# Optimization experiments

Measured on AMD Instinct MI355X. Metric: run time of the kernel, lower is better.

The kernel has to match this reference:

```python
import jax, jax.numpy as jnp
import numpy as np

D = 512; NH = 8; FF = 2048; LE = 6; LD = 6; V = 97; SM = 512; SQ = 128; B = 16
EPS = 1e-5


def _posenc(length, depth):
    half = depth // 2
    pos = jnp.arange(length, dtype=jnp.float32)[:, None]
    dep = jnp.arange(half, dtype=jnp.float32)[None, :] / half
    ang = pos / (10000.0 ** dep)
    return jnp.concatenate([jnp.sin(ang), jnp.cos(ang)], axis=-1)  # [length, depth]


def _ln(x, w, b):
    mu = jnp.mean(x, axis=-1, keepdims=True)
    var = jnp.mean((x - mu) ** 2, axis=-1, keepdims=True)
    return (x - mu) * jax.lax.rsqrt(var + EPS) * w + b


def _heads(t, S, Bt):
    return t.reshape(S, Bt * NH, D // NH).transpose(1, 0, 2)  # [B*H, S, dk]


def _self_attn(x, wqkv, bqkv, wo, bo, causal):
    S, Bt, _ = x.shape
    qkv = x @ wqkv.T + bqkv
    q, k, v = jnp.split(qkv, 3, axis=-1)
    q = _heads(q, S, Bt); k = _heads(k, S, Bt); v = _heads(v, S, Bt)
    scores = jnp.einsum('hqd,hkd->hqk', q, k) / jnp.sqrt(jnp.asarray(D // NH, x.dtype))
    if causal:
        mask = jnp.triu(jnp.ones((S, S), bool), 1)
        scores = jnp.where(mask[None], -jnp.inf, scores)
    attn = jax.nn.softmax(scores, axis=-1)
    out = jnp.einsum('hqk,hkd->hqd', attn, v).transpose(1, 0, 2).reshape(S, Bt, D)
    return out @ wo.T + bo


def _cross_attn(query, memory, wq, bq, wk, bk, wv, bv, wo, bo):
    Sq, Bt, _ = query.shape
    Sm = memory.shape[0]
    q = _heads(query @ wq.T + bq, Sq, Bt)
    k = _heads(memory @ wk.T + bk, Sm, Bt)
    v = _heads(memory @ wv.T + bv, Sm, Bt)
    scores = jnp.einsum('hqd,hkd->hqk', q, k) / jnp.sqrt(jnp.asarray(D // NH, query.dtype))
    attn = jax.nn.softmax(scores, axis=-1)
    out = jnp.einsum('hqk,hkd->hqd', attn, v).transpose(1, 0, 2).reshape(Sq, Bt, D)
    return out @ wo.T + bo


def _forward(src, tokens, tok_emb,
             enc_qkv_w, enc_qkv_b, enc_out_w, enc_out_b,
             enc_l1_w, enc_l1_b, enc_l2_w, enc_l2_b,
             enc_n1_w, enc_n1_b, enc_n2_w, enc_n2_b,
             dec_qkv_w, dec_qkv_b, dec_sout_w, dec_sout_b,
             dec_q_w, dec_q_b, dec_k_w, dec_k_b, dec_v_w, dec_v_b,
             dec_cout_w, dec_cout_b,
             dec_l1_w, dec_l1_b, dec_l2_w, dec_l2_b,
             dec_n1_w, dec_n1_b, dec_n2_w, dec_n2_b, dec_n3_w, dec_n3_b,
             out_w, out_b):
    # ---- encoder ----
    x = src  # [SM, B, D]
    for i in range(LE):
        x2 = _self_attn(x, enc_qkv_w[i], enc_qkv_b[i], enc_out_w[i], enc_out_b[i], causal=False)
        x = _ln(x + x2, enc_n1_w[i], enc_n1_b[i])
        x2 = jax.nn.relu(x @ enc_l1_w[i].T + enc_l1_b[i]) @ enc_l2_w[i].T + enc_l2_b[i]
        x = _ln(x + x2, enc_n2_w[i], enc_n2_b[i])
    memory = x
    # ---- decoder ----
    tgt = tok_emb[tokens] + _posenc(tokens.shape[0], D)[:, None, :]  # [SQ, B, D]
    for i in range(LD):
        x2 = _self_attn(tgt, dec_qkv_w[i], dec_qkv_b[i], dec_sout_w[i], dec_sout_b[i], causal=True)
        tgt = _ln(tgt + x2, dec_n1_w[i], dec_n1_b[i])
        x2 = _cross_attn(tgt, memory, dec_q_w[i], dec_q_b[i], dec_k_w[i], dec_k_b[i],
                         dec_v_w[i], dec_v_b[i], dec_cout_w[i], dec_cout_b[i])
        tgt = _ln(tgt + x2, dec_n2_w[i], dec_n2_b[i])
        x2 = jax.nn.relu(tgt @ dec_l1_w[i].T + dec_l1_b[i]) @ dec_l2_w[i].T + dec_l2_b[i]
        tgt = _ln(tgt + x2, dec_n3_w[i], dec_n3_b[i])
    return tgt @ out_w.T + out_b  # [SQ, B, V]


def setup_inputs() -> dict:
    key = jax.random.key(0)
    ks = iter(jax.random.split(key, 64))
    g = lambda shape: jax.random.normal(next(ks), shape, dtype=jnp.float32) * 0.02
    inp = {
        'src': jax.random.normal(next(ks), (SM, B, D), dtype=jnp.float32),
        'tokens': jax.random.randint(next(ks), (SQ, B), 0, V),
        'tok_emb': g((V, D)),
        'enc_qkv_w': g((LE, 3 * D, D)), 'enc_qkv_b': g((LE, 3 * D)),
        'enc_out_w': g((LE, D, D)), 'enc_out_b': g((LE, D)),
        'enc_l1_w': g((LE, FF, D)), 'enc_l1_b': g((LE, FF)),
        'enc_l2_w': g((LE, D, FF)), 'enc_l2_b': g((LE, D)),
        'enc_n1_w': jnp.ones((LE, D)), 'enc_n1_b': jnp.zeros((LE, D)),
        'enc_n2_w': jnp.ones((LE, D)), 'enc_n2_b': jnp.zeros((LE, D)),
        'dec_qkv_w': g((LD, 3 * D, D)), 'dec_qkv_b': g((LD, 3 * D)),
        'dec_sout_w': g((LD, D, D)), 'dec_sout_b': g((LD, D)),
        'dec_q_w': g((LD, D, D)), 'dec_q_b': g((LD, D)),
        'dec_k_w': g((LD, D, D)), 'dec_k_b': g((LD, D)),
        'dec_v_w': g((LD, D, D)), 'dec_v_b': g((LD, D)),
        'dec_cout_w': g((LD, D, D)), 'dec_cout_b': g((LD, D)),
        'dec_l1_w': g((LD, FF, D)), 'dec_l1_b': g((LD, FF)),
        'dec_l2_w': g((LD, D, FF)), 'dec_l2_b': g((LD, D)),
        'dec_n1_w': jnp.ones((LD, D)), 'dec_n1_b': jnp.zeros((LD, D)),
        'dec_n2_w': jnp.ones((LD, D)), 'dec_n2_b': jnp.zeros((LD, D)),
        'dec_n3_w': jnp.ones((LD, D)), 'dec_n3_b': jnp.zeros((LD, D)),
        'out_w': g((V, D)), 'out_b': g((V,)),
    }
    return inp


def reference(src, tokens, tok_emb,
              enc_qkv_w, enc_qkv_b, enc_out_w, enc_out_b,
              enc_l1_w, enc_l1_b, enc_l2_w, enc_l2_b,
              enc_n1_w, enc_n1_b, enc_n2_w, enc_n2_b,
              dec_qkv_w, dec_qkv_b, dec_sout_w, dec_sout_b,
              dec_q_w, dec_q_b, dec_k_w, dec_k_b, dec_v_w, dec_v_b,
              dec_cout_w, dec_cout_b,
              dec_l1_w, dec_l1_b, dec_l2_w, dec_l2_b,
              dec_n1_w, dec_n1_b, dec_n2_w, dec_n2_b, dec_n3_w, dec_n3_b,
              out_w, out_b):
    return _forward(src, tokens, tok_emb,
                    enc_qkv_w, enc_qkv_b, enc_out_w, enc_out_b,
                    enc_l1_w, enc_l1_b, enc_l2_w, enc_l2_b,
                    enc_n1_w, enc_n1_b, enc_n2_w, enc_n2_b,
                    dec_qkv_w, dec_qkv_b, dec_sout_w, dec_sout_b,
                    dec_q_w, dec_q_b, dec_k_w, dec_k_b, dec_v_w, dec_v_b,
                    dec_cout_w, dec_cout_b,
                    dec_l1_w, dec_l1_b, dec_l2_w, dec_l2_b,
                    dec_n1_w, dec_n1_b, dec_n2_w, dec_n2_b, dec_n3_w, dec_n3_b,
                    out_w, out_b)
```

## Files before the change

### kernel.cpp

```cpp
#include <hip/hip_runtime.h>
#include <hip/hip_bf16.h>
#include <cstddef>
#include <cstdint>

#define D_MODEL 512
#define BATCH 16
#define EPS_LN 1e-5f

typedef __bf16 bf16x8 __attribute__((ext_vector_type(8)));
typedef float f32x4 __attribute__((ext_vector_type(4)));
typedef unsigned short u16x8 __attribute__((ext_vector_type(8)));
typedef unsigned short u16x4 __attribute__((ext_vector_type(4)));
typedef unsigned short u16x2 __attribute__((ext_vector_type(2)));

__device__ __forceinline__ void gload_lds16(const void* g, void* l) {
    __builtin_amdgcn_global_load_lds(
        (const __attribute__((address_space(1))) void*)g,
        (__attribute__((address_space(3))) void*)l,
        16, 0, 0);
}

template <int BM, int OUTBF16>
__global__ __launch_bounds__(256) void gemm_mfma(
    const __bf16* __restrict__ A, const __bf16* __restrict__ W,
    const float* __restrict__ bias, const float* __restrict__ bias2,
    int bsplit, void* __restrict__ Cout, int N, int M, int K, int relu)
{
    constexpr int WC     = (BM == 128) ? 2 : 4;
    constexpr int WSPAN  = 128 / WC;
    constexpr int NC     = WSPAN / 16;
    constexpr int ABYTES = BM * 128;
    constexpr int PA     = ABYTES / 4096;
    constexpr int BUFB   = ABYTES + 16384;

    __shared__ __align__(16) char smem[2 * BUFB];

    const int tid  = threadIdx.x;
    const int lane = tid & 63;
    const int wid  = tid >> 6;
    const int wrow = (BM == 128) ? (wid >> 1) : 0;
    const int wcol = (BM == 128) ? (wid & 1) : wid;
    const int row0 = blockIdx.y * BM;
    const int col0 = blockIdx.x * 128;

    const int lrow  = lane & 15;
    const int lhalf = lane >> 4;
    const int koff0 = ((lhalf) ^ (lrow & 7)) * 16;
    const int koff1 = ((4 + lhalf) ^ (lrow & 7)) * 16;

    const int srow = tid >> 3;
    const int slot = tid & 7;
    const int sg   = slot ^ (srow & 7);

    f32x4 acc[4][NC] = {};

    const __bf16* Abase = A + (size_t)(row0 + srow) * K + sg * 8;
    const __bf16* Wbase = W + (size_t)(col0 + srow) * K + sg * 8;

    auto stage = [&](char* buf, int kt) {
#pragma unroll
        for (int p = 0; p < PA; ++p)
            gload_lds16(Abase + (size_t)p * 32 * K + kt, buf + p * 4096 + tid * 16);
#pragma unroll
        for (int p = 0; p < 4; ++p)
            gload_lds16(Wbase + (size_t)p * 32 * K + kt,
                        buf + ABYTES + p * 4096 + tid * 16);
    };

    stage(smem, 0);
    const int nkt = K >> 6;
    int cur = 0;
    for (int kt = 0; kt < nkt; ++kt) {
        __syncthreads();
        if (kt + 1 < nkt) stage(smem + (cur ^ 1) * BUFB, (kt + 1) * 64);
        const char* aB = smem + cur * BUFB + (wrow * 64 + lrow) * 128;
        const char* wB = smem + cur * BUFB + ABYTES + (wcol * WSPAN + lrow) * 128;
#pragma unroll
        for (int ks = 0; ks < 2; ++ks) {
            const int ko = ks ? koff1 : koff0;
            bf16x8 af[4], bfr[NC];
#pragma unroll
            for (int m = 0; m < 4; ++m) af[m]  = *(const bf16x8*)(aB + m * 2048 + ko);
#pragma unroll
            for (int n = 0; n < NC; ++n) bfr[n] = *(const bf16x8*)(wB + n * 2048 + ko);
#pragma unroll
            for (int m = 0; m < 4; ++m)
#pragma unroll
                for (int n = 0; n < NC; ++n)
                    acc[m][n] = __builtin_amdgcn_mfma_f32_16x16x32_bf16(
                        af[m], bfr[n], acc[m][n], 0, 0, 0);
        }
        cur ^= 1;
    }

    const int orow = row0 + wrow * 64 + lhalf * 4;
    const int ocol = col0 + wcol * WSPAN + lrow;
#pragma unroll
    for (int n = 0; n < NC; ++n) {
        const int c = ocol + n * 16;
        if (c < M) {
            const float bv = (bias2 && c >= bsplit) ? bias2[c - bsplit] : bias[c];
#pragma unroll
            for (int m = 0; m < 4; ++m) {
#pragma unroll
                for (int j = 0; j < 4; ++j) {
                    const int r = orow + m * 16 + j;
                    float v = acc[m][n][j] + bv;
                    if (relu) v = fmaxf(v, 0.f);
                    if (OUTBF16) ((__bf16*)Cout)[(size_t)r * M + c] = (__bf16)v;
                    else         ((float*)Cout)[(size_t)r * M + c] = v;
                }
            }
        }
    }
}

__global__ __launch_bounds__(256) void transpose_v(
    const __bf16* __restrict__ V, __bf16* __restrict__ VT,
    int stride, int voff, int S)
{
    __shared__ __align__(16) char smem[8192];
    const int tid = threadIdx.x;
    const int kc = blockIdx.x, h = blockIdx.y, b = blockIdx.z;
    const int srow = tid >> 3, slot = tid & 7;
#pragma unroll
    for (int p = 0; p < 2; ++p) {
        int r = p * 32 + srow;
        const __bf16* src = V + ((size_t)(kc * 64 + r) * BATCH + b) * stride
                              + voff + h * 64 + slot * 8;
        gload_lds16(src, smem + (p * 256 + tid) * 16);
    }
    __syncthreads();
    const int l = tid & 63, w = tid >> 6;
    const int d2 = w * 8 + (l >> 3);
    const int s0 = (l & 7) * 8;
    unsigned rows[8];
#pragma unroll
    for (int e = 0; e < 8; ++e)
        rows[e] = *(const unsigned*)(smem + (s0 + e) * 128 + d2 * 4);
    union { __bf16 h8[8]; u16x8 u; } r0, r1;
#pragma unroll
    for (int e = 0; e < 8; ++e) {
        r0.h8[e] = ((const __bf16*)&rows[e])[0];
        r1.h8[e] = ((const __bf16*)&rows[e])[1];
    }
    size_t obase = ((size_t)(b * 8 + h) * 64 + d2 * 2) * S + kc * 64 + s0;
    *(u16x8*)(VT + obase)     = r0.u;
    *(u16x8*)(VT + obase + S) = r1.u;
}

template <int CAUSAL>
__global__ __launch_bounds__(256) void attn_mfma(
    const __bf16* __restrict__ Qb, const __bf16* __restrict__ Kb,
    const __bf16* __restrict__ VT, __bf16* __restrict__ Op,
    int Skv, int qstride, int kstride, int koff, float scale)
{
    __shared__ __align__(16) char smem[40960];
    const int tid = threadIdx.x;
    const int l   = tid & 63;
    const int w   = tid >> 6;
    char* Psm = smem + 32768 + w * 2048;

    const int qc = blockIdx.x;
    const int h  = blockIdx.y;
    const int b  = blockIdx.z;
    const int l15 = l & 15;
    const int g   = l >> 4;
    const int sw  = l15 & 7;

    const int sq = qc * 64 + w * 16 + l15;
    const __bf16* qrow = Qb + ((size_t)sq * BATCH + b) * qstride + h * 64 + g * 8;
    const bf16x8 qf0 = *(const bf16x8*)(qrow);
    const bf16x8 qf1 = *(const bf16x8*)(qrow + 32);

    const int srow = tid >> 3;
    const int slot = tid & 7;

    auto stageKV = [&](char* buf, int kc) {
#pragma unroll
        for (int p = 0; p < 2; ++p) {
            const int r   = p * 32 + srow;
            const int sgo = (slot ^ (r & 7)) * 8;
            const __bf16* ksrc = Kb + ((size_t)(kc * 64 + r) * BATCH + b) * kstride
                                    + koff + h * 64 + sgo;
            gload_lds16(ksrc, buf + (p * 256 + tid) * 16);
            const __bf16* vsrc = VT + ((size_t)((b * 8 + h) * 64 + r)) * Skv
                                    + kc * 64 + sgo;
            gload_lds16(vsrc, buf + 8192 + (p * 256 + tid) * 16);
        }
    };

    f32x4 acc[4] = {};
    float m_run = -1e30f, l_run = 0.f;

    const int nkc = CAUSAL ? (qc + 1) : (Skv >> 6);
    stageKV(smem, 0);
    int cur = 0;
    for (int kc = 0; kc < nkc; ++kc) {
        __syncthreads();
        if (kc + 1 < nkc) stageKV(smem + (cur ^ 1) * 16384, kc + 1);
        const char* Ksm = smem + cur * 16384;
        const char* Vsm = Ksm + 8192;

        f32x4 st[4];
#pragma unroll
        for (int f = 0; f < 4; ++f) {
            const char* kr = Ksm + (f * 16 + l15) * 128;
            bf16x8 ka0 = *(const bf16x8*)(kr + ((g ^ sw) * 16));
            bf16x8 ka1 = *(const bf16x8*)(kr + (((4 + g) ^ sw) * 16));
            f32x4 z = {};
            z = __builtin_amdgcn_mfma_f32_16x16x32_bf16(ka0, qf0, z, 0, 0, 0);
            st[f] = __builtin_amdgcn_mfma_f32_16x16x32_bf16(ka1, qf1, z, 0, 0, 0);
        }

        float rmax = -1e30f;
#pragma unroll
        for (int f = 0; f < 4; ++f)
#pragma unroll
            for (int j = 0; j < 4; ++j) {
                float v = st[f][j] * scale;
                if (CAUSAL) {
                    if (kc * 64 + f * 16 + g * 4 + j > sq) v = -1e30f;
                }
                st[f][j] = v;
                rmax = fmaxf(rmax, v);
            }
        rmax = fmaxf(rmax, __shfl_xor(rmax, 16, 64));
        rmax = fmaxf(rmax, __shfl_xor(rmax, 32, 64));
        const float mn = fmaxf(m_run, rmax);
        const float corr = __expf(m_run - mn);
        m_run = mn;
        float rsum = 0.f;
#pragma unroll
        for (int f = 0; f < 4; ++f)
#pragma unroll
            for (int j = 0; j < 4; ++j) {
                float p = __expf(st[f][j] - mn);
                st[f][j] = p;
                rsum += p;
            }
        rsum += __shfl_xor(rsum, 16, 64);
        rsum += __shfl_xor(rsum, 32, 64);
        l_run = l_run * corr + rsum;

#pragma unroll
        for (int j = 0; j < 4; ++j) {
            const float cj = __shfl(corr, g * 20 + j, 64);
            acc[0][j] *= cj; acc[1][j] *= cj; acc[2][j] *= cj; acc[3][j] *= cj;
        }

#pragma unroll
        for (int f = 0; f < 4; ++f)
#pragma unroll
            for (int j2 = 0; j2 < 2; ++j2) {
                union { __bf16 h2[2]; unsigned u; } cv;
                cv.h2[0] = (__bf16)st[f][2 * j2];
                cv.h2[1] = (__bf16)st[f][2 * j2 + 1];
                const int key0 = 16 * f + 4 * g + 2 * j2;
                const int byte = l15 * 128 + (((key0 >> 3) ^ sw) * 16) + (key0 & 7) * 2;
                *(unsigned*)(Psm + byte) = cv.u;
            }

#pragma unroll
        for (int ks = 0; ks < 2; ++ks) {
            const int so = ((4 * ks + g) ^ sw) * 16;
            bf16x8 pa = *(const bf16x8*)(Psm + l15 * 128 + so);
#pragma unroll
            for (int n = 0; n < 4; ++n) {
                bf16x8 vb = *(const bf16x8*)(Vsm + (n * 16 + l15) * 128 + so);
                acc[n] = __builtin_amdgcn_mfma_f32_16x16x32_bf16(pa, vb, acc[n], 0, 0, 0);
            }
        }
        cur ^= 1;
    }

    const float inv = 1.f / l_run;
#pragma unroll
    for (int j = 0; j < 4; ++j) {
        const float ij = __shfl(inv, g * 20 + j, 64);
        const int s = qc * 64 + w * 16 + g * 4 + j;
        __bf16* orow = Op + ((size_t)s * BATCH + b) * D_MODEL + h * 64 + l15;
#pragma unroll
        for (int n = 0; n < 4; ++n)
            orow[n * 16] = (__bf16)(acc[n][j] * ij);
    }
}

__global__ __launch_bounds__(256) void add_ln(
    const float* __restrict__ X, const __bf16* __restrict__ Y,
    const float* __restrict__ w, const float* __restrict__ bias,
    float* __restrict__ Of, __bf16* __restrict__ Oh)
{
    const int t   = blockIdx.x;
    const int tid = threadIdx.x;
    const float2 x2 = *(const float2*)(X + (size_t)t * D_MODEL + tid * 2);
    const u16x2 yv = *(const u16x2*)(Y + (size_t)t * D_MODEL + tid * 2);
    union { u16x2 u; __bf16 h2[2]; } yc; yc.u = yv;
    float v0 = x2.x + (float)yc.h2[0], v1 = x2.y + (float)yc.h2[1];
    float sum = v0 + v1;
    float sq  = v0 * v0 + v1 * v1;
#pragma unroll
    for (int off = 32; off; off >>= 1) {
        sum += __shfl_xor(sum, off);
        sq  += __shfl_xor(sq, off);
    }
    __shared__ float ssum[4], ssq[4];
    const int wid = tid >> 6;
    if ((tid & 63) == 0) { ssum[wid] = sum; ssq[wid] = sq; }
    __syncthreads();
    sum = ssum[0] + ssum[1] + ssum[2] + ssum[3];
    sq  = ssq[0] + ssq[1] + ssq[2] + ssq[3];

    const float mu  = sum * (1.f / D_MODEL);
    const float var = sq * (1.f / D_MODEL) - mu * mu;
    const float rs  = rsqrtf(var + EPS_LN);
    const float2 w2 = *(const float2*)(w + tid * 2);
    const float2 b2 = *(const float2*)(bias + tid * 2);
    float o0 = (v0 - mu) * rs * w2.x + b2.x;
    float o1 = (v1 - mu) * rs * w2.y + b2.y;
    *(float2*)(Of + (size_t)t * D_MODEL + tid * 2) = make_float2(o0, o1);
    union { __bf16 h2[2]; u16x2 u; } cv;
    cv.h2[0] = (__bf16)o0; cv.h2[1] = (__bf16)o1;
    *(u16x2*)(Oh + (size_t)t * D_MODEL + tid * 2) = cv.u;
}

__global__ __launch_bounds__(256) void embed_pos(
    const int* __restrict__ tokens, const float* __restrict__ emb,
    float* __restrict__ Of, __bf16* __restrict__ Oh)
{
    const int t   = blockIdx.x;
    const int s   = t / BATCH;
    const int tid = threadIdx.x;
    const int tok = tokens[t];
    const float C = 9.210340371976184f / 256.f;
    const int d = tid * 2;
    const int j = (d < 256) ? d : (d - 256);
    float a0 = (float)s * expf(-(float)j * C);
    float a1 = (float)s * expf(-(float)(j + 1) * C);
    float pe0 = (d < 256) ? sinf(a0) : cosf(a0);
    float pe1 = (d < 256) ? sinf(a1) : cosf(a1);
    const float2 e2 = *(const float2*)(emb + (size_t)tok * D_MODEL + d);
    float o0 = e2.x + pe0, o1 = e2.y + pe1;
    *(float2*)(Of + (size_t)t * D_MODEL + d) = make_float2(o0, o1);
    union { __bf16 h2[2]; u16x2 u; } cv;
    cv.h2[0] = (__bf16)o0; cv.h2[1] = (__bf16)o1;
    *(u16x2*)(Oh + (size_t)t * D_MODEL + d) = cv.u;
}

struct CvtSeg { const float* s; __bf16* d; int n8; };
struct CvtArgs { CvtSeg seg[8]; int tot8; };

__global__ __launch_bounds__(256) void cvt_multi(CvtArgs a)
{
    const int stride = gridDim.x * 256;
    for (int u = blockIdx.x * 256 + threadIdx.x; u < a.tot8; u += stride) {
        int v = u;
        for (int sgi = 0; sgi < 8; ++sgi) {
            const int n8 = a.seg[sgi].n8;
            if (v < n8) {
                const float4 f0 = ((const float4*)a.seg[sgi].s)[v * 2];
                const float4 f1 = ((const float4*)a.seg[sgi].s)[v * 2 + 1];
                union { __bf16 h[8]; u16x8 u; } c;
                c.h[0] = (__bf16)f0.x; c.h[1] = (__bf16)f0.y;
                c.h[2] = (__bf16)f0.z; c.h[3] = (__bf16)f0.w;
                c.h[4] = (__bf16)f1.x; c.h[5] = (__bf16)f1.y;
                c.h[6] = (__bf16)f1.z; c.h[7] = (__bf16)f1.w;
                ((u16x8*)a.seg[sgi].d)[v] = c.u;
                break;
            }
            v -= n8;
        }
    }
}

__global__ __launch_bounds__(256) void pad_outw(
    const float* __restrict__ w, __bf16* __restrict__ o)
{
    const int idx = blockIdx.x * 256 + threadIdx.x;
    const int r = idx >> 9;
    const int c = idx & 511;
    o[idx] = (__bf16)(r < 97 ? w[r * 512 + c] : 0.f);
}

extern "C" void kernel_launch(void* const* d_in, const int* in_sizes, int n_in,
                              void* d_out, int out_size, void* d_ws, size_t ws_size,
                              hipStream_t stream)
{
    const float* src     = (const float*)d_in[0];
    const int*   tokens  = (const int*)d_in[1];
    const float* tok_emb = (const float*)d_in[2];
    const float* enc_qkv_w = (const float*)d_in[3];
    const float* enc_qkv_b = (const float*)d_in[4];
    const float* enc_out_w = (const float*)d_in[5];
    const float* enc_out_b = (const float*)d_in[6];
    const float* enc_l1_w  = (const float*)d_in[7];
    const float* enc_l1_b  = (const float*)d_in[8];
    const float* enc_l2_w  = (const float*)d_in[9];
    const float* enc_l2_b  = (const float*)d_in[10];
    const float* enc_n1_w  = (const float*)d_in[11];
    const float* enc_n1_b  = (const float*)d_in[12];
    const float* enc_n2_w  = (const float*)d_in[13];
    const float* enc_n2_b  = (const float*)d_in[14];
    const float* dec_qkv_w = (const float*)d_in[15];
    const float* dec_qkv_b = (const float*)d_in[16];
    const float* dec_sout_w = (const float*)d_in[17];
    const float* dec_sout_b = (const float*)d_in[18];
    const float* dec_q_w   = (const float*)d_in[19];
    const float* dec_q_b   = (const float*)d_in[20];
    const float* dec_k_w   = (const float*)d_in[21];
    const float* dec_k_b   = (const float*)d_in[22];
    const float* dec_v_w   = (const float*)d_in[23];
    const float* dec_v_b   = (const float*)d_in[24];
    const float* dec_cout_w = (const float*)d_in[25];
    const float* dec_cout_b = (const float*)d_in[26];
    const float* dec_l1_w  = (const float*)d_in[27];
    const float* dec_l1_b  = (const float*)d_in[28];
    const float* dec_l2_w  = (const float*)d_in[29];
    const float* dec_l2_b  = (const float*)d_in[30];
    const float* dec_n1_w  = (const float*)d_in[31];
    const float* dec_n1_b  = (const float*)d_in[32];
    const float* dec_n2_w  = (const float*)d_in[33];
    const float* dec_n2_b  = (const float*)d_in[34];
    const float* dec_n3_w  = (const float*)d_in[35];
    const float* dec_n3_b  = (const float*)d_in[36];
    const float* out_w     = (const float*)d_in[37];
    const float* out_b     = (const float*)d_in[38];

    const int NE = 512 * BATCH;
    const int ND = 128 * BATCH;
    const float scale = 0.125f;

    char* w8 = (char*)d_ws;
    float*  Ax_f = (float*) (w8 + 0);
    float*  T_f  = (float*) (w8 + 16777216);
    __bf16* Ax_h = (__bf16*)(w8 + 20971520);
    __bf16* T_h  = (__bf16*)(w8 + 29360128);
    __bf16* AO_h = (__bf16*)(w8 + 31457280);
    __bf16* Wk   = (__bf16*)(w8 + 39845888);
    __bf16* OWp  = (__bf16*)(w8 + 49283072);
    __bf16* VT   = (__bf16*)(w8 + 49414144);
    char*   Gb   = w8 + 57802752;
    __bf16* Gqkv = (__bf16*)Gb;
    __bf16* Gh   = (__bf16*)Gb;
    __bf16* Gq   = (__bf16*)Gb;
    __bf16* Gkv  = (__bf16*)(Gb + 2097152);
    __bf16* Y_h  = (__bf16*)(w8 + 91357184);

    auto gemm = [&](const __bf16* Am, const __bf16* Wm, const float* bv,
                    const float* bv2, int bsplit, void* C,
                    int N, int M, int K, int relu, bool outbf) {
        const int nb128 = ((M + 127) / 128) * (N / 128);
        if (nb128 >= 256) {
            dim3 grid((M + 127) / 128, N / 128);
            if (outbf) gemm_mfma<128, 1><<<grid, 256, 0, stream>>>(Am, Wm, bv, bv2, bsplit, C, N, M, K, relu);
            else       gemm_mfma<128, 0><<<grid, 256, 0, stream>>>(Am, Wm, bv, bv2, bsplit, C, N, M, K, relu);
        } else {
            dim3 grid((M + 127) / 128, N / 64);
            if (outbf) gemm_mfma<64, 1><<<grid, 256, 0, stream>>>(Am, Wm, bv, bv2, bsplit, C, N, M, K, relu);
            else       gemm_mfma<64, 0><<<grid, 256, 0, stream>>>(Am, Wm, bv, bv2, bsplit, C, N, M, K, relu);
        }
    };
    auto cvt = [&](CvtArgs& a) {
        int tot = 0;
        for (int i = 0; i < 8; ++i) tot += a.seg[i].n8;
        a.tot8 = tot;
        cvt_multi<<<1024, 256, 0, stream>>>(a);
    };

    { CvtArgs a = {}; a.seg[0] = { src, Ax_h, NE * 512 / 8 }; cvt(a); }

    __bf16* wqkv = Wk;
    __bf16* wout = Wk + 786432;
    __bf16* wl1  = Wk + 1048576;
    __bf16* wl2  = Wk + 2097152;
    for (int i = 0; i < 6; ++i) {
        CvtArgs a = {};
        a.seg[0] = { enc_qkv_w + (size_t)i * 786432,  wqkv, 786432 / 8 };
        a.seg[1] = { enc_out_w + (size_t)i * 262144,  wout, 262144 / 8 };
        a.seg[2] = { enc_l1_w  + (size_t)i * 1048576, wl1, 1048576 / 8 };
        a.seg[3] = { enc_l2_w  + (size_t)i * 1048576, wl2, 1048576 / 8 };
        cvt(a);

        gemm(Ax_h, wqkv, enc_qkv_b + (size_t)i * 1536, nullptr, 0, Gqkv, NE, 1536, 512, 0, true);
        transpose_v<<<dim3(8, 8, BATCH), 256, 0, stream>>>(Gqkv, VT, 1536, 1024, 512);
        attn_mfma<0><<<dim3(8, 8, BATCH), 256, 0, stream>>>(
            Gqkv, Gqkv, VT, AO_h, 512, 1536, 1536, 512, scale);
        gemm(AO_h, wout, enc_out_b + (size_t)i * 512, nullptr, 0, Y_h, NE, 512, 512, 0, true);
        add_ln<<<NE, 256, 0, stream>>>((i == 0) ? src : Ax_f, Y_h,
                                       enc_n1_w + (size_t)i * 512, enc_n1_b + (size_t)i * 512,
                                       Ax_f, Ax_h);
        gemm(Ax_h, wl1, enc_l1_b + (size_t)i * 2048, nullptr, 0, Gh, NE, 2048, 512, 1, true);
        gemm(Gh, wl2, enc_l2_b + (size_t)i * 512, nullptr, 0, Y_h, NE, 512, 2048, 0, true);
        add_ln<<<NE, 256, 0, stream>>>(Ax_f, Y_h,
                                       enc_n2_w + (size_t)i * 512, enc_n2_b + (size_t)i * 512,
                                       Ax_f, Ax_h);
    }

    embed_pos<<<ND, 256, 0, stream>>>(tokens, tok_emb, T_f, T_h);
    __bf16* dqkv = Wk;
    __bf16* dsout = Wk + 786432;
    __bf16* dq   = Wk + 1048576;
    __bf16* dkv  = Wk + 1310720;
    __bf16* dcout = Wk + 1835008;
    __bf16* dl1  = Wk + 2097152;
    __bf16* dl2  = Wk + 3145728;
    for (int i = 0; i < 6; ++i) {
        CvtArgs a = {};
        a.seg[0] = { dec_qkv_w  + (size_t)i * 786432,  dqkv,  786432 / 8 };
        a.seg[1] = { dec_sout_w + (size_t)i * 262144,  dsout, 262144 / 8 };
        a.seg[2] = { dec_q_w    + (size_t)i * 262144,  dq,    262144 / 8 };
        a.seg[3] = { dec_k_w    + (size_t)i * 262144,  dkv,   262144 / 8 };
        a.seg[4] = { dec_v_w    + (size_t)i * 262144,  dkv + 262144, 262144 / 8 };
        a.seg[5] = { dec_cout_w + (size_t)i * 262144,  dcout, 262144 / 8 };
        a.seg[6] = { dec_l1_w   + (size_t)i * 1048576, dl1,  1048576 / 8 };
        a.seg[7] = { dec_l2_w   + (size_t)i * 1048576, dl2,  1048576 / 8 };
        cvt(a);

        gemm(T_h, dqkv, dec_qkv_b + (size_t)i * 1536, nullptr, 0, Gqkv, ND, 1536, 512, 0, true);
        transpose_v<<<dim3(2, 8, BATCH), 256, 0, stream>>>(Gqkv, VT, 1536, 1024, 128);
        attn_mfma<1><<<dim3(2, 8, BATCH), 256, 0, stream>>>(
            Gqkv, Gqkv, VT, AO_h, 128, 1536, 1536, 512, scale);
        gemm(AO_h, dsout, dec_sout_b + (size_t)i * 512, nullptr, 0, Y_h, ND, 512, 512, 0, true);
        add_ln<<<ND, 256, 0, stream>>>(T_f, Y_h,
                                       dec_n1_w + (size_t)i * 512, dec_n1_b + (size_t)i * 512,
                                       T_f, T_h);
        gemm(T_h,  dq, dec_q_b + (size_t)i * 512, nullptr, 0, Gq, ND, 512, 512, 0, true);
        gemm(Ax_h, dkv, dec_k_b + (size_t)i * 512, dec_v_b + (size_t)i * 512, 512,
             Gkv, NE, 1024, 512, 0, true);
        transpose_v<<<dim3(8, 8, BATCH), 256, 0, stream>>>(Gkv, VT, 1024, 512, 512);
        attn_mfma<0><<<dim3(2, 8, BATCH), 256, 0, stream>>>(
            Gq, Gkv, VT, AO_h, 512, 512, 1024, 0, scale);
        gemm(AO_h, dcout, dec_cout_b + (size_t)i * 512, nullptr, 0, Y_h, ND, 512, 512, 0, true);
        add_ln<<<ND, 256, 0, stream>>>(T_f, Y_h,
                                       dec_n2_w + (size_t)i * 512, dec_n2_b + (size_t)i * 512,
                                       T_f, T_h);
        gemm(T_h, dl1, dec_l1_b + (size_t)i * 2048, nullptr, 0, Gh, ND, 2048, 512, 1, true);
        gemm(Gh, dl2, dec_l2_b + (size_t)i * 512, nullptr, 0, Y_h, ND, 512, 2048, 0, true);
        add_ln<<<ND, 256, 0, stream>>>(T_f, Y_h,
                                       dec_n3_w + (size_t)i * 512, dec_n3_b + (size_t)i * 512,
                                       T_f, T_h);
    }

    pad_outw<<<256, 256, 0, stream>>>(out_w, OWp);
    gemm(T_h, OWp, out_b, nullptr, 0, (float*)d_out, ND, 97, 512, 0, false);
}
```

Before: 1.654 ms.

## Switch to batch-major activations, fuse V transpose into GEMM epilogue, upfront weight conversion

Activations move from sequence-major to batch-major token order, with permute_src and embed_pos producing the new order and the final GEMM permuting rows back. The standalone transpose_v kernels go away: the QKV and KV GEMMs write V directly in transposed layout from their epilogue. Decoder K and V weights are read from separate buffers inside the GEMM. Most GEMMs use a swapped-operand MFMA path so the epilogue can do vectorized row-contiguous stores. All weights are converted to bf16 in one launch at the start when the workspace is large enough, replacing the per-layer conversions, at the cost of more workspace and a strided transposed-V store.

After: 1.652 ms. No clear change (-0.1%).

```diff
diff --git a/kernel.cpp b/kernel.cpp
--- a/kernel.cpp
+++ b/kernel.cpp
@@ -20,11 +20,13 @@
         16, 0, 0);
 }
 
-template <int BM, int OUTBF16>
+template <int BM, int OUTBF16, int SWAP>
 __global__ __launch_bounds__(256) void gemm_mfma(
     const __bf16* __restrict__ A, const __bf16* __restrict__ W,
-    const float* __restrict__ bias, const float* __restrict__ bias2,
-    int bsplit, void* __restrict__ Cout, int N, int M, int K, int relu)
+    const __bf16* __restrict__ W2, int wsplit,
+    const float* __restrict__ bias, const float* __restrict__ bias2, int bsplit,
+    void* __restrict__ Cout, __bf16* __restrict__ VTout, int m_vt0, int log2S,
+    int N, int Mlim, int MS, int K, int relu, int permrow)
 {
     constexpr int WC     = (BM == 128) ? 2 : 4;
     constexpr int WSPAN  = 128 / WC;
@@ -54,8 +56,12 @@
 
     f32x4 acc[4][NC] = {};
 
+    const __bf16* Wsel = W;
+    int wc0 = col0;
+    if (col0 >= wsplit) { Wsel = W2; wc0 = col0 - wsplit; }
+
     const __bf16* Abase = A + (size_t)(row0 + srow) * K + sg * 8;
-    const __bf16* Wbase = W + (size_t)(col0 + srow) * K + sg * 8;
+    const __bf16* Wbase = Wsel + (size_t)(wc0 + srow) * K + sg * 8;
 
     auto stage = [&](char* buf, int kt) {
 #pragma unroll
@@ -83,77 +89,95 @@
             for (int m = 0; m < 4; ++m) af[m]  = *(const bf16x8*)(aB + m * 2048 + ko);
 #pragma unroll
             for (int n = 0; n < NC; ++n) bfr[n] = *(const bf16x8*)(wB + n * 2048 + ko);
-#pragma unroll
-            for (int m = 0; m < 4; ++m)
-#pragma unroll
-                for (int n = 0; n < NC; ++n)
-                    acc[m][n] = __builtin_amdgcn_mfma_f32_16x16x32_bf16(
-                        af[m], bfr[n], acc[m][n], 0, 0, 0);
+            if (SWAP) {
+#pragma unroll
+                for (int m = 0; m < 4; ++m)
+#pragma unroll
+                    for (int n = 0; n < NC; ++n)
+                        acc[m][n] = __builtin_amdgcn_mfma_f32_16x16x32_bf16(
+                            bfr[n], af[m], acc[m][n], 0, 0, 0);
+            } else {
+#pragma unroll
+                for (int m = 0; m < 4; ++m)
+#pragma unroll
+                    for (int n = 0; n < NC; ++n)
+                        acc[m][n] = __builtin_amdgcn_mfma_f32_16x16x32_bf16(
+                            af[m], bfr[n], acc[m][n], 0, 0, 0);
+            }
         }
         cur ^= 1;
     }
 
-    const int orow = row0 + wrow * 64 + lhalf * 4;
-    const int ocol = col0 + wcol * WSPAN + lrow;
-#pragma unroll
-    for (int n = 0; n < NC; ++n) {
-        const int c = ocol + n * 16;
-        if (c < M) {
-            const float bv = (bias2 && c >= bsplit) ? bias2[c - bsplit] : bias[c];
-#pragma unroll
-            for (int m = 0; m < 4; ++m) {
-#pragma unroll
-                for (int j = 0; j < 4; ++j) {
-                    const int r = orow + m * 16 + j;
-                    float v = acc[m][n][j] + bv;
-                    if (relu) v = fmaxf(v, 0.f);
-                    if (OUTBF16) ((__bf16*)Cout)[(size_t)r * M + c] = (__bf16)v;
-                    else         ((float*)Cout)[(size_t)r * M + c] = v;
+    if (SWAP) {
+#pragma unroll
+        for (int m = 0; m < 4; ++m) {
+            const int r = row0 + wrow * 64 + m * 16 + lrow;
+#pragma unroll
+            for (int n = 0; n < NC; ++n) {
+                const int c0 = col0 + wcol * WSPAN + n * 16 + lhalf * 4;
+                const float4 bv = *(const float4*)(bias + c0);
+                float o0 = acc[m][n][0] + bv.x, o1 = acc[m][n][1] + bv.y;
+                float o2 = acc[m][n][2] + bv.z, o3 = acc[m][n][3] + bv.w;
+                if (relu) {
+                    o0 = fmaxf(o0, 0.f); o1 = fmaxf(o1, 0.f);
+                    o2 = fmaxf(o2, 0.f); o3 = fmaxf(o3, 0.f);
                 }
-            }
-        }
-    }
-}
-
-__global__ __launch_bounds__(256) void transpose_v(
-    const __bf16* __restrict__ V, __bf16* __restrict__ VT,
-    int stride, int voff, int S)
-{
-    __shared__ __align__(16) char smem[8192];
-    const int tid = threadIdx.x;
-    const int kc = blockIdx.x, h = blockIdx.y, b = blockIdx.z;
-    const int srow = tid >> 3, slot = tid & 7;
-#pragma unroll
-    for (int p = 0; p < 2; ++p) {
-        int r = p * 32 + srow;
-        const __bf16* src = V + ((size_t)(kc * 64 + r) * BATCH + b) * stride
-                              + voff + h * 64 + slot * 8;
-        gload_lds16(src, smem + (p * 256 + tid) * 16);
-    }
-    __syncthreads();
-    const int l = tid & 63, w = tid >> 6;
-    const int d2 = w * 8 + (l >> 3);
-    const int s0 = (l & 7) * 8;
-    unsigned rows[8];
-#pragma unroll
-    for (int e = 0; e < 8; ++e)
-        rows[e] = *(const unsigned*)(smem + (s0 + e) * 128 + d2 * 4);
-    union { __bf16 h8[8]; u16x8 u; } r0, r1;
-#pragma unroll
-    for (int e = 0; e < 8; ++e) {
-        r0.h8[e] = ((const __bf16*)&rows[e])[0];
-        r1.h8[e] = ((const __bf16*)&rows[e])[1];
-    }
-    size_t obase = ((size_t)(b * 8 + h) * 64 + d2 * 2) * S + kc * 64 + s0;
-    *(u16x8*)(VT + obase)     = r0.u;
-    *(u16x8*)(VT + obase + S) = r1.u;
+                if (OUTBF16) {
+                    union { __bf16 h4[4]; u16x4 u; } pk;
+                    pk.h4[0] = (__bf16)o0; pk.h4[1] = (__bf16)o1;
+                    pk.h4[2] = (__bf16)o2; pk.h4[3] = (__bf16)o3;
+                    *(u16x4*)((__bf16*)Cout + (size_t)r * MS + c0) = pk.u;
+                } else {
+                    *(float4*)((float*)Cout + (size_t)r * MS + c0) =
+                        make_float4(o0, o1, o2, o3);
+                }
+            }
+        }
+    } else {
+        const int orow = row0 + wrow * 64 + lhalf * 4;
+        const int ocol = col0 + wcol * WSPAN + lrow;
+        const int smask = (1 << log2S) - 1;
+#pragma unroll
+        for (int n = 0; n < NC; ++n) {
+            const int c = ocol + n * 16;
+            if (c >= m_vt0) {
+                const int cv = c - m_vt0;
+                const int hh = cv >> 6, dd = cv & 63;
+                const float bv = (bias2 && c >= bsplit) ? bias2[c - bsplit] : bias[c];
+#pragma unroll
+                for (int m = 0; m < 4; ++m) {
+                    const int rr = orow + m * 16;
+                    const int bb = rr >> log2S, ss = rr & smask;
+                    union { __bf16 h4[4]; u16x4 u; } pk;
+#pragma unroll
+                    for (int j = 0; j < 4; ++j)
+                        pk.h4[j] = (__bf16)(acc[m][n][j] + bv);
+                    *(u16x4*)(VTout + (((size_t)((bb * 8 + hh) * 64 + dd)) << log2S) + ss) = pk.u;
+                }
+            } else if (c < Mlim) {
+                const float bv = (bias2 && c >= bsplit) ? bias2[c - bsplit] : bias[c];
+#pragma unroll
+                for (int m = 0; m < 4; ++m) {
+#pragma unroll
+                    for (int j = 0; j < 4; ++j) {
+                        int rr = orow + m * 16 + j;
+                        if (permrow) rr = ((rr & smask) * BATCH) + (rr >> log2S);
+                        float v = acc[m][n][j] + bv;
+                        if (relu) v = fmaxf(v, 0.f);
+                        if (OUTBF16) ((__bf16*)Cout)[(size_t)rr * MS + c] = (__bf16)v;
+                        else         ((float*)Cout)[(size_t)rr * MS + c] = v;
+                    }
+                }
+            }
+        }
+    }
 }
 
 template <int CAUSAL>
 __global__ __launch_bounds__(256) void attn_mfma(
     const __bf16* __restrict__ Qb, const __bf16* __restrict__ Kb,
     const __bf16* __restrict__ VT, __bf16* __restrict__ Op,
-    int Skv, int qstride, int kstride, int koff, float scale)
+    int Sq, int Skv, int qstride, int kstride, int koff, float scale)
 {
     __shared__ __align__(16) char smem[40960];
     const int tid = threadIdx.x;
@@ -169,7 +193,7 @@
     const int sw  = l15 & 7;
 
     const int sq = qc * 64 + w * 16 + l15;
-    const __bf16* qrow = Qb + ((size_t)sq * BATCH + b) * qstride + h * 64 + g * 8;
+    const __bf16* qrow = Qb + ((size_t)(b * Sq + sq)) * qstride + h * 64 + g * 8;
     const bf16x8 qf0 = *(const bf16x8*)(qrow);
     const bf16x8 qf1 = *(const bf16x8*)(qrow + 32);
 
@@ -181,7 +205,7 @@
         for (int p = 0; p < 2; ++p) {
             const int r   = p * 32 + srow;
             const int sgo = (slot ^ (r & 7)) * 8;
-            const __bf16* ksrc = Kb + ((size_t)(kc * 64 + r) * BATCH + b) * kstride
+            const __bf16* ksrc = Kb + ((size_t)(b * Skv + kc * 64 + r)) * kstride
                                     + koff + h * 64 + sgo;
             gload_lds16(ksrc, buf + (p * 256 + tid) * 16);
             const __bf16* vsrc = VT + ((size_t)((b * 8 + h) * 64 + r)) * Skv
@@ -279,7 +303,7 @@
     for (int j = 0; j < 4; ++j) {
         const float ij = __shfl(inv, g * 20 + j, 64);
         const int s = qc * 64 + w * 16 + g * 4 + j;
-        __bf16* orow = Op + ((size_t)s * BATCH + b) * D_MODEL + h * 64 + l15;
+        __bf16* orow = Op + ((size_t)(b * Sq + s)) * D_MODEL + h * 64 + l15;
 #pragma unroll
         for (int n = 0; n < 4; ++n)
             orow[n * 16] = (__bf16)(acc[n][j] * ij);
@@ -324,14 +348,27 @@
     *(u16x2*)(Oh + (size_t)t * D_MODEL + tid * 2) = cv.u;
 }
 
+__global__ __launch_bounds__(256) void permute_src(
+    const float* __restrict__ src, float* __restrict__ Of, __bf16* __restrict__ Oh)
+{
+    const int t = blockIdx.x;
+    const int b = t >> 9, s = t & 511;
+    const int tid = threadIdx.x;
+    const float2 v = *(const float2*)(src + ((size_t)(s * BATCH + b)) * D_MODEL + tid * 2);
+    *(float2*)(Of + (size_t)t * D_MODEL + tid * 2) = v;
+    union { __bf16 h2[2]; u16x2 u; } cv;
+    cv.h2[0] = (__bf16)v.x; cv.h2[1] = (__bf16)v.y;
+    *(u16x2*)(Oh + (size_t)t * D_MODEL + tid * 2) = cv.u;
+}
+
 __global__ __launch_bounds__(256) void embed_pos(
     const int* __restrict__ tokens, const float* __restrict__ emb,
     float* __restrict__ Of, __bf16* __restrict__ Oh)
 {
     const int t   = blockIdx.x;
-    const int s   = t / BATCH;
+    const int b   = t >> 7, s = t & 127;
     const int tid = threadIdx.x;
-    const int tok = tokens[t];
+    const int tok = tokens[s * BATCH + b];
     const float C = 9.210340371976184f / 256.f;
     const int d = tid * 2;
     const int j = (d < 256) ? d : (d - 256);
@@ -348,14 +385,14 @@
 }
 
 struct CvtSeg { const float* s; __bf16* d; int n8; };
-struct CvtArgs { CvtSeg seg[8]; int tot8; };
+struct CvtArgs { CvtSeg seg[12]; int tot8; };
 
 __global__ __launch_bounds__(256) void cvt_multi(CvtArgs a)
 {
     const int stride = gridDim.x * 256;
     for (int u = blockIdx.x * 256 + threadIdx.x; u < a.tot8; u += stride) {
         int v = u;
-        for (int sgi = 0; sgi < 8; ++sgi) {
+        for (int sgi = 0; sgi < 12; ++sgi) {
             const int n8 = a.seg[sgi].n8;
             if (v < n8) {
                 const float4 f0 = ((const float4*)a.seg[sgi].s)[v * 2];
@@ -429,6 +466,7 @@
     const int NE = 512 * BATCH;
     const int ND = 128 * BATCH;
     const float scale = 0.125f;
+    const int BIG = 1 << 30;
 
     char* w8 = (char*)d_ws;
     float*  Ax_f = (float*) (w8 + 0);
@@ -436,111 +474,179 @@
     __bf16* Ax_h = (__bf16*)(w8 + 20971520);
     __bf16* T_h  = (__bf16*)(w8 + 29360128);
     __bf16* AO_h = (__bf16*)(w8 + 31457280);
-    __bf16* Wk   = (__bf16*)(w8 + 39845888);
-    __bf16* OWp  = (__bf16*)(w8 + 49283072);
-    __bf16* VT   = (__bf16*)(w8 + 49414144);
-    char*   Gb   = w8 + 57802752;
-    __bf16* Gqkv = (__bf16*)Gb;
+    __bf16* Y_h  = (__bf16*)(w8 + 39845888);
+    __bf16* VT   = (__bf16*)(w8 + 48234496);
+    __bf16* OWp  = (__bf16*)(w8 + 56623104);
+    char*   Gb   = w8 + 56754176;
+    __bf16* Gqk  = (__bf16*)Gb;
     __bf16* Gh   = (__bf16*)Gb;
     __bf16* Gq   = (__bf16*)Gb;
-    __bf16* Gkv  = (__bf16*)(Gb + 2097152);
-    __bf16* Y_h  = (__bf16*)(w8 + 91357184);
-
-    auto gemm = [&](const __bf16* Am, const __bf16* Wm, const float* bv,
-                    const float* bv2, int bsplit, void* C,
-                    int N, int M, int K, int relu, bool outbf) {
+    __bf16* Gk   = (__bf16*)(Gb + 2097152);
+    __bf16* WB   = (__bf16*)(w8 + 90308608);
+
+    const bool upfront = ws_size >= (size_t)178388992;
+
+    auto gemmS = [&](const __bf16* Am, const __bf16* Wm, const float* bv,
+                     void* C, int N, int M, int K, int relu) {
+        const int nb128 = (M / 128) * (N / 128);
+        if (nb128 >= 256) {
+            dim3 grid(M / 128, N / 128);
+            gemm_mfma<128, 1, 1><<<grid, 256, 0, stream>>>(
+                Am, Wm, nullptr, BIG, bv, nullptr, 0, C, nullptr, BIG, 0,
+                N, M, M, K, relu, 0);
+        } else {
+            dim3 grid(M / 128, N / 64);
+            gemm_mfma<64, 1, 1><<<grid, 256, 0, stream>>>(
+                Am, Wm, nullptr, BIG, bv, nullptr, 0, C, nullptr, BIG, 0,
+                N, M, M, K, relu, 0);
+        }
+    };
+    auto gemmN = [&](const __bf16* Am, const __bf16* Wm, const __bf16* W2m, int wsplit,
+                     const float* bv, const float* bv2, int bsplit,
+                     void* C, __bf16* VTp, int m_vt0, int log2S,
+                     int N, int M, int MS, int K, bool outbf, int permrow) {
         const int nb128 = ((M + 127) / 128) * (N / 128);
         if (nb128 >= 256) {
             dim3 grid((M + 127) / 128, N / 128);
-            if (outbf) gemm_mfma<128, 1><<<grid, 256, 0, stream>>>(Am, Wm, bv, bv2, bsplit, C, N, M, K, relu);
-            else       gemm_mfma<128, 0><<<grid, 256, 0, stream>>>(Am, Wm, bv, bv2, bsplit, C, N, M, K, relu);
+            if (outbf) gemm_mfma<128, 1, 0><<<grid, 256, 0, stream>>>(
+                Am, Wm, W2m, wsplit, bv, bv2, bsplit, C, VTp, m_vt0, log2S,
+                N, M, MS, K, 0, permrow);
+            else       gemm_mfma<128, 0, 0><<<grid, 256, 0, stream>>>(
+                Am, Wm, W2m, wsplit, bv, bv2, bsplit, C, VTp, m_vt0, log2S,
+                N, M, MS, K, 0, permrow);
         } else {
             dim3 grid((M + 127) / 128, N / 64);
-            if (outbf) gemm_mfma<64, 1><<<grid, 256, 0, stream>>>(Am, Wm, bv, bv2, bsplit, C, N, M, K, relu);
-            else       gemm_mfma<64, 0><<<grid, 256, 0, stream>>>(Am, Wm, bv, bv2, bsplit, C, N, M, K, relu);
+            if (outbf) gemm_mfma<64, 1, 0><<<grid, 256, 0, stream>>>(
+                Am, Wm, W2m, wsplit, bv, bv2, bsplit, C, VTp, m_vt0, log2S,
+                N, M, MS, K, 0, permrow);
+            else       gemm_mfma<64, 0, 0><<<grid, 256, 0, stream>>>(
+                Am, Wm, W2m, wsplit, bv, bv2, bsplit, C, VTp, m_vt0, log2S,
+                N, M, MS, K, 0, permrow);
         }
     };
-    auto cvt = [&](CvtArgs& a) {
+    auto cvt = [&](CvtArgs& a, int blocks) {
         int tot = 0;
-        for (int i = 0; i < 8; ++i) tot += a.seg[i].n8;
+        for (int i = 0; i < 12; ++i) tot += a.seg[i].n8;
         a.tot8 = tot;
-        cvt_multi<<<1024, 256, 0, stream>>>(a);
+        cvt_multi<<<blocks, 256, 0, stream>>>(a);
     };
 
-    { CvtArgs a = {}; a.seg[0] = { src, Ax_h, NE * 512 / 8 }; cvt(a); }
-
-    __bf16* wqkv = Wk;
-    __bf16* wout = Wk + 786432;
-    __bf16* wl1  = Wk + 1048576;
-    __bf16* wl2  = Wk + 2097152;
+    permute_src<<<NE, 256, 0, stream>>>(src, Ax_f, Ax_h);
+    pad_outw<<<256, 256, 0, stream>>>(out_w, OWp);
+
+    __bf16* WencQKV = WB;
+    __bf16* WencOUT = WencQKV + 4718592;
+    __bf16* WencL1  = WencOUT + 1572864;
+    __bf16* WencL2  = WencL1 + 6291456;
+    __bf16* WdecQKV = WencL2 + 6291456;
+    __bf16* WdecSOUT = WdecQKV + 4718592;
+    __bf16* WdecQ   = WdecSOUT + 1572864;
+    __bf16* WdecK   = WdecQ + 1572864;
+    __bf16* WdecV   = WdecK + 1572864;
+    __bf16* WdecCOUT = WdecV + 1572864;
+    __bf16* WdecL1  = WdecCOUT + 1572864;
+    __bf16* WdecL2  = WdecL1 + 6291456;
+
+    if (upfront) {
+        CvtArgs a = {};
+        a.seg[0]  = { enc_qkv_w,  WencQKV,  4718592 / 8 };
+        a.seg[1]  = { enc_out_w,  WencOUT,  1572864 / 8 };
+        a.seg[2]  = { enc_l1_w,   WencL1,   6291456 / 8 };
+        a.seg[3]  = { enc_l2_w,   WencL2,   6291456 / 8 };
+        a.seg[4]  = { dec_qkv_w,  WdecQKV,  4718592 / 8 };
+        a.seg[5]  = { dec_sout_w, WdecSOUT, 1572864 / 8 };
+        a.seg[6]  = { dec_q_w,    WdecQ,    1572864 / 8 };
+        a.seg[7]  = { dec_k_w,    WdecK,    1572864 / 8 };
+        a.seg[8]  = { dec_v_w,    WdecV,    1572864 / 8 };
+        a.seg[9]  = { dec_cout_w, WdecCOUT, 1572864 / 8 };
+        a.seg[10] = { dec_l1_w,   WdecL1,   6291456 / 8 };
+        a.seg[11] = { dec_l2_w,   WdecL2,   6291456 / 8 };
+        cvt(a, 2048);
+    }
+
     for (int i = 0; i < 6; ++i) {
-        CvtArgs a = {};
-        a.seg[0] = { enc_qkv_w + (size_t)i * 786432,  wqkv, 786432 / 8 };
-        a.seg[1] = { enc_out_w + (size_t)i * 262144,  wout, 262144 / 8 };
-        a.seg[2] = { enc_l1_w  + (size_t)i * 1048576, wl1, 1048576 / 8 };
-        a.seg[3] = { enc_l2_w  + (size_t)i * 1048576, wl2, 1048576 / 8 };
-        cvt(a);
-
-        gemm(Ax_h, wqkv, enc_qkv_b + (size_t)i * 1536, nullptr, 0, Gqkv, NE, 1536, 512, 0, true);
-        transpose_v<<<dim3(8, 8, BATCH), 256, 0, stream>>>(Gqkv, VT, 1536, 1024, 512);
+        __bf16 *wqkv, *wout, *wl1, *wl2;
+        if (upfront) {
+            wqkv = WencQKV + (size_t)i * 786432;
+            wout = WencOUT + (size_t)i * 262144;
+            wl1  = WencL1 + (size_t)i * 1048576;
+            wl2  = WencL2 + (size_t)i * 1048576;
+        } else {
+            wqkv = WB; wout = WB + 786432; wl1 = WB + 1048576; wl2 = WB + 2097152;
+            CvtArgs a = {};
+            a.seg[0] = { enc_qkv_w + (size_t)i * 786432,  wqkv, 786432 / 8 };
+            a.seg[1] = { enc_out_w + (size_t)i * 262144,  wout, 262144 / 8 };
+            a.seg[2] = { enc_l1_w  + (size_t)i * 1048576, wl1, 1048576 / 8 };
+            a.seg[3] = { enc_l2_w  + (size_t)i * 1048576, wl2, 1048576 / 8 };
+            cvt(a, 1024);
+        }
+
+        gemmN(Ax_h, wqkv, nullptr, BIG, enc_qkv_b + (size_t)i * 1536, nullptr, 0,
+              Gqk, VT, 1024, 9, NE, 1536, 1024, 512, true, 0);
         attn_mfma<0><<<dim3(8, 8, BATCH), 256, 0, stream>>>(
-            Gqkv, Gqkv, VT, AO_h, 512, 1536, 1536, 512, scale);
-        gemm(AO_h, wout, enc_out_b + (size_t)i * 512, nullptr, 0, Y_h, NE, 512, 512, 0, true);
-        add_ln<<<NE, 256, 0, stream>>>((i == 0) ? src : Ax_f, Y_h,
+            Gqk, Gqk, VT, AO_h, 512, 512, 1024, 1024, 512, scale);
+        gemmS(AO_h, wout, enc_out_b + (size_t)i * 512, Y_h, NE, 512, 512, 0);
+        add_ln<<<NE, 256, 0, stream>>>(Ax_f, Y_h,
                                        enc_n1_w + (size_t)i * 512, enc_n1_b + (size_t)i * 512,
                                        Ax_f, Ax_h);
-        gemm(Ax_h, wl1, enc_l1_b + (size_t)i * 2048, nullptr, 0, Gh, NE, 2048, 512, 1, true);
-        gemm(Gh, wl2, enc_l2_b + (size_t)i * 512, nullptr, 0, Y_h, NE, 512, 2048, 0, true);
+        gemmS(Ax_h, wl1, enc_l1_b + (size_t)i * 2048, Gh, NE, 2048, 512, 1);
+        gemmS(Gh, wl2, enc_l2_b + (size_t)i * 512, Y_h, NE, 512, 2048, 0);
         add_ln<<<NE, 256, 0, stream>>>(Ax_f, Y_h,
                                        enc_n2_w + (size_t)i * 512, enc_n2_b + (size_t)i * 512,
                                        Ax_f, Ax_h);
     }
 
     embed_pos<<<ND, 256, 0, stream>>>(tokens, tok_emb, T_f, T_h);
-    __bf16* dqkv = Wk;
-    __bf16* dsout = Wk + 786432;
-    __bf16* dq   = Wk + 1048576;
-    __bf16* dkv  = Wk + 1310720;
-    __bf16* dcout = Wk + 1835008;
-    __bf16* dl1  = Wk + 2097152;
-    __bf16* dl2  = Wk + 3145728;
     for (int i = 0; i < 6; ++i) {
-        CvtArgs a = {};
-        a.seg[0] = { dec_qkv_w  + (size_t)i * 786432,  dqkv,  786432 / 8 };
-        a.seg[1] = { dec_sout_w + (size_t)i * 262144,  dsout, 262144 / 8 };
-        a.seg[2] = { dec_q_w    + (size_t)i * 262144,  dq,    262144 / 8 };
-        a.seg[3] = { dec_k_w    + (size_t)i * 262144,  dkv,   262144 / 8 };
-        a.seg[4] = { dec_v_w    + (size_t)i * 262144,  dkv + 262144, 262144 / 8 };
-        a.seg[5] = { dec_cout_w + (size_t)i * 262144,  dcout, 262144 / 8 };
-        a.seg[6] = { dec_l1_w   + (size_t)i * 1048576, dl1,  1048576 / 8 };
-        a.seg[7] = { dec_l2_w   + (size_t)i * 1048576, dl2,  1048576 / 8 };
-        cvt(a);
-
-        gemm(T_h, dqkv, dec_qkv_b + (size_t)i * 1536, nullptr, 0, Gqkv, ND, 1536, 512, 0, true);
-        transpose_v<<<dim3(2, 8, BATCH), 256, 0, stream>>>(Gqkv, VT, 1536, 1024, 128);
+        __bf16 *dqkv, *dsout, *dq, *dk, *dv, *dcout, *dl1, *dl2;
+        if (upfront) {
+            dqkv  = WdecQKV + (size_t)i * 786432;
+            dsout = WdecSOUT + (size_t)i * 262144;
+            dq    = WdecQ + (size_t)i * 262144;
+            dk    = WdecK + (size_t)i * 262144;
+            dv    = WdecV + (size_t)i * 262144;
+            dcout = WdecCOUT + (size_t)i * 262144;
+            dl1   = WdecL1 + (size_t)i * 1048576;
+            dl2   = WdecL2 + (size_t)i * 1048576;
+        } else {
+            dqkv = WB; dsout = WB + 786432; dq = WB + 1048576; dk = WB + 1310720;
+            dv = WB + 1572864; dcout = WB + 1835008; dl1 = WB + 2097152; dl2 = WB + 3145728;
+            CvtArgs a = {};
+            a.seg[0] = { dec_qkv_w  + (size_t)i * 786432,  dqkv,  786432 / 8 };
+            a.seg[1] = { dec_sout_w + (size_t)i * 262144,  dsout, 262144 / 8 };
+            a.seg[2] = { dec_q_w    + (size_t)i * 262144,  dq,    262144 / 8 };
+            a.seg[3] = { dec_k_w    + (size_t)i * 262144,  dk,    262144 / 8 };
+            a.seg[4] = { dec_v_w    + (size_t)i * 262144,  dv,    262144 / 8 };
+            a.seg[5] = { dec_cout_w + (size_t)i * 262144,  dcout, 262144 / 8 };
+            a.seg[6] = { dec_l1_w   + (size_t)i * 1048576, dl1,  1048576 / 8 };
+            a.seg[7] = { dec_l2_w   + (size_t)i * 1048576, dl2,  1048576 / 8 };
+            cvt(a, 1024);
+        }
+
+        gemmN(T_h, dqkv, nullptr, BIG, dec_qkv_b + (size_t)i * 1536, nullptr, 0,
+              Gqk, VT, 1024, 7, ND, 1536, 1024, 512, true, 0);
         attn_mfma<1><<<dim3(2, 8, BATCH), 256, 0, stream>>>(
-            Gqkv, Gqkv, VT, AO_h, 128, 1536, 1536, 512, scale);
-        gemm(AO_h, dsout, dec_sout_b + (size_t)i * 512, nullptr, 0, Y_h, ND, 512, 512, 0, true);
+            Gqk, Gqk, VT, AO_h, 128, 128, 1024, 1024, 512, scale);
+        gemmS(AO_h, dsout, dec_sout_b + (size_t)i * 512, Y_h, ND, 512, 512, 0);
         add_ln<<<ND, 256, 0, stream>>>(T_f, Y_h,
                                        dec_n1_w + (size_t)i * 512, dec_n1_b + (size_t)i * 512,
                                        T_f, T_h);
-        gemm(T_h,  dq, dec_q_b + (size_t)i * 512, nullptr, 0, Gq, ND, 512, 512, 0, true);
-        gemm(Ax_h, dkv, dec_k_b + (size_t)i * 512, dec_v_b + (size_t)i * 512, 512,
-             Gkv, NE, 1024, 512, 0, true);
-        transpose_v<<<dim3(8, 8, BATCH), 256, 0, stream>>>(Gkv, VT, 1024, 512, 512);
+        gemmS(T_h, dq, dec_q_b + (size_t)i * 512, Gq, ND, 512, 512, 0);
+        gemmN(Ax_h, dk, dv, 512, dec_k_b + (size_t)i * 512, dec_v_b + (size_t)i * 512, 512,
+              Gk, VT, 512, 9, NE, 1024, 512, 512, true, 0);
         attn_mfma<0><<<dim3(2, 8, BATCH), 256, 0, stream>>>(
-            Gq, Gkv, VT, AO_h, 512, 512, 1024, 0, scale);
-        gemm(AO_h, dcout, dec_cout_b + (size_t)i * 512, nullptr, 0, Y_h, ND, 512, 512, 0, true);
+            Gq, Gk, VT, AO_h, 128, 512, 512, 512, 0, scale);
+        gemmS(AO_h, dcout, dec_cout_b + (size_t)i * 512, Y_h, ND, 512, 512, 0);
         add_ln<<<ND, 256, 0, stream>>>(T_f, Y_h,
                                        dec_n2_w + (size_t)i * 512, dec_n2_b + (size_t)i * 512,
                                        T_f, T_h);
-        gemm(T_h, dl1, dec_l1_b + (size_t)i * 2048, nullptr, 0, Gh, ND, 2048, 512, 1, true);
-        gemm(Gh, dl2, dec_l2_b + (size_t)i * 512, nullptr, 0, Y_h, ND, 512, 2048, 0, true);
+        gemmS(T_h, dl1, dec_l1_b + (size_t)i * 2048, Gh, ND, 2048, 512, 1);
+        gemmS(Gh, dl2, dec_l2_b + (size_t)i * 512, Y_h, ND, 512, 2048, 0);
         add_ln<<<ND, 256, 0, stream>>>(T_f, Y_h,
                                        dec_n3_w + (size_t)i * 512, dec_n3_b + (size_t)i * 512,
                                        T_f, T_h);
     }
 
-    pad_outw<<<256, 256, 0, stream>>>(out_w, OWp);
-    gemm(T_h, OWp, out_b, nullptr, 0, (float*)d_out, ND, 97, 512, 0, false);
-}
+    gemmN(T_h, OWp, nullptr, BIG, out_b, nullptr, 0,
+          (float*)d_out, nullptr, BIG, 7, ND, 97, 97, 512, false, 1);
+}
```
